# Kernel optimization log

Hardware: AMD Instinct MI355X
Metric: run time of the kernel (lower is better)

The kernel has to match this reference:

```python
import jax, jax.numpy as jnp
import numpy as np

N, E = 50000, 800000
D = 64          # output_dim == d_s == d_e
H = 128         # psi hidden width
PSI_IN = 2 * D + 2 * D + D  # 320


def setup_inputs() -> dict:
    key = jax.random.key(0)
    ks = jax.random.split(key, 12)
    scale = lambda fan_in: 1.0 / np.sqrt(fan_in)
    return {
        "h_d_prev": jax.random.normal(ks[0], (N, D), jnp.float32),
        "h_s": jax.random.normal(ks[1], (N, D), jnp.float32),
        "edge_feat": jax.random.normal(ks[2], (E, D), jnp.float32),
        "sender": jax.random.randint(ks[3], (E,), 0, N, jnp.int32),
        "receiver": jax.random.randint(ks[4], (E,), 0, N, jnp.int32),
        # psi MLP params (all layers use relu, incl. last: final_activation=None)
        "W0": jax.random.normal(ks[5], (PSI_IN, H), jnp.float32) * scale(PSI_IN),
        "b0": jnp.zeros((H,), jnp.float32),
        "W1": jax.random.normal(ks[6], (H, H), jnp.float32) * scale(H),
        "b1": jnp.zeros((H,), jnp.float32),
        "W2": jax.random.normal(ks[7], (H, D), jnp.float32) * scale(H),
        "b2": jnp.zeros((D,), jnp.float32),
        # final linear transform W (no bias)
        "Wm": jax.random.normal(ks[8], (D, D), jnp.float32) * scale(D),
    }


def reference(h_d_prev, h_s, edge_feat, sender, receiver, W0, b0, W1, b1, W2, b2, Wm):
    # gather node feats to edges
    h_di = h_d_prev[sender]      # [E, D]
    h_dj = h_d_prev[receiver]    # [E, D]
    h_si = h_s[sender]           # [E, D]
    h_sj = h_s[receiver]         # [E, D]
    psi_in = jnp.concatenate([h_si, h_sj, h_di, h_dj, edge_feat], axis=-1)  # [E, 320]
    # psi MLP: relu on every layer (final_activation=None keeps default relu)
    x = jax.nn.relu(psi_in @ W0 + b0)
    x = jax.nn.relu(x @ W1 + b1)
    psi = jax.nn.relu(x @ W2 + b2)          # [E, D]
    s_ij = psi * (h_dj - h_di)              # [E, D]
    agg = jax.ops.segment_sum(s_ij, receiver, num_segments=h_d_prev.shape[0])  # [N, D]
    return h_d_prev + agg @ Wm
```

## Files before the change

kernel.cpp:

```cpp
#include <hip/hip_runtime.h>

#define NN   50000
#define EE   800000
#define DD   64
#define HH   128
#define KIN  320
#define TILE_E 64

typedef __bf16 bf16x8 __attribute__((ext_vector_type(8)));
typedef float  f32x4  __attribute__((ext_vector_type(4)));

#if __has_builtin(__builtin_amdgcn_cvt_pk_bf16_f32)
typedef __bf16 bf16x2_t __attribute__((ext_vector_type(2)));
__device__ __forceinline__ unsigned int pk2(float a, float b) {
  union { bf16x2_t v; unsigned int u; } cv;
  cv.v = __builtin_amdgcn_cvt_pk_bf16_f32(a, b);
  return cv.u;
}
__device__ __forceinline__ unsigned short f2bf(float a) {
  return (unsigned short)(pk2(a, a) & 0xFFFFu);
}
#else
__device__ __forceinline__ unsigned short f2bf(float f) {
  union { float f; unsigned int u; } v; v.f = f;
  unsigned int u = v.u + 0x7FFFu + ((v.u >> 16) & 1u);
  return (unsigned short)(u >> 16);
}
__device__ __forceinline__ unsigned int pk2(float a, float b) {
  return (unsigned int)f2bf(a) | ((unsigned int)f2bf(b) << 16);
}
#endif

__device__ __forceinline__ float bf2f(unsigned short b) {
  union { unsigned int u; float f; } v; v.u = ((unsigned int)b) << 16; return v.f;
}

__device__ __forceinline__ int psiIdx(int row, int kk) {
  return ((((row >> 4) * 10 + (kk >> 5)) << 6) + ((row & 15) << 2) + ((kk >> 3) & 3)) * 8
         + (kk & 7);
}

__global__ __launch_bounds__(256) void prep_weights(
    const float* __restrict__ W0,
    const float* __restrict__ W1,
    const float* __restrict__ W2,
    unsigned short* __restrict__ WT0,
    unsigned short* __restrict__ WT1,
    unsigned short* __restrict__ WT2) {
  int t = blockIdx.x * 256 + threadIdx.x;
  if (t < KIN * HH) {
    int k = t / HH, n = t % HH;
    WT0[n * KIN + k] = f2bf(W0[t]);
  } else if (t < KIN * HH + HH * HH) {
    int u = t - KIN * HH; int k = u / HH, n = u % HH;
    WT1[n * HH + k] = f2bf(W1[u]);
  } else {
    int u = t - KIN * HH - HH * HH; int k = u / DD, n = u % DD;
    WT2[n * HH + k] = f2bf(W2[u]);
  }
}

__global__ __launch_bounds__(256) void prep_tables(
    const float* __restrict__ hd, const float* __restrict__ hs,
    unsigned short* __restrict__ hdb, unsigned short* __restrict__ hsb) {
  int t = blockIdx.x * 256 + threadIdx.x;
  const int n = NN * DD / 8;
  const float* src; unsigned short* dst; int i;
  if (t < n) { src = hd; dst = hdb; i = t; }
  else       { src = hs; dst = hsb; i = t - n; }
  float4 a = *(const float4*)(src + (size_t)i * 8);
  float4 b = *(const float4*)(src + (size_t)i * 8 + 4);
  uint4 w;
  w.x = pk2(a.x, a.y); w.y = pk2(a.z, a.w);
  w.z = pk2(b.x, b.y); w.w = pk2(b.z, b.w);
  *(uint4*)(dst + (size_t)i * 8) = w;
}

__global__ __launch_bounds__(256, 4) void edge_mlp(
    const unsigned short* __restrict__ hdb,
    const unsigned short* __restrict__ hsb,
    const float* __restrict__ ef,
    const int* __restrict__ snd,
    const int* __restrict__ rcv,
    const unsigned short* __restrict__ WT0,
    const float* __restrict__ b0,
    const unsigned short* __restrict__ WT1,
    const float* __restrict__ b1,
    const unsigned short* __restrict__ WT2,
    const float* __restrict__ b2,
    float* __restrict__ agg)
{
  __shared__ __align__(16) unsigned short psi[TILE_E * KIN];

  const int tid  = threadIdx.x;
  const int e0   = blockIdx.x * TILE_E;
  const int wv   = tid >> 6;
  const int lane = tid & 63;
  const int ln   = lane & 15;
  const int quad = lane >> 4;

  int ridx[16];
  #pragma unroll
  for (int mt = 0; mt < 4; ++mt)
    #pragma unroll
    for (int i = 0; i < 4; ++i)
      ridx[mt * 4 + i] = rcv[e0 + mt * 16 + quad * 4 + i];

  #pragma unroll
  for (int i = 0; i < 10; ++i) {
    const int seg = i >> 1;
    int e = ((i << 5) + (tid >> 3)) & 63;
    int c = tid & 7;
    int unit = (((e >> 4) * 10 + seg * 2 + (c >> 2)) << 6) + ((e & 15) << 2) + (c & 3);
    uint4 w;
    if (seg < 4) {
      const unsigned short* tb = (seg & 2) ? hdb : hsb;
      const int* ix = (seg & 1) ? rcv : snd;
      w = *(const uint4*)(tb + (size_t)ix[e0 + e] * DD + c * 8);
    } else {
      const float* src = ef + (size_t)(e0 + e) * DD;
      float4 v0 = *(const float4*)(src + c * 8);
      float4 v1 = *(const float4*)(src + c * 8 + 4);
      w.x = pk2(v0.x, v0.y); w.y = pk2(v0.z, v0.w);
      w.z = pk2(v1.x, v1.y); w.w = pk2(v1.z, v1.w);
    }
    *(uint4*)(&psi[unit * 8]) = w;
  }
  __syncthreads();

  f32x4 acc0[4], acc1[4];

  {
    #pragma unroll
    for (int m = 0; m < 4; ++m) { acc0[m] = (f32x4){0,0,0,0}; acc1[m] = (f32x4){0,0,0,0}; }
    const unsigned short* wb0 = WT0 + (wv * 32 + ln) * KIN + quad * 8;
    const unsigned short* wb1 = wb0 + 16 * KIN;
    #pragma unroll
    for (int k0 = 0; k0 < 10; ++k0) {
      bf16x8 bf0 = *(const bf16x8*)(wb0 + k0 * 32);
      bf16x8 bf1 = *(const bf16x8*)(wb1 + k0 * 32);
      #pragma unroll
      for (int mt = 0; mt < 4; ++mt) {
        bf16x8 af = *(const bf16x8*)(&psi[(((mt * 10 + k0) << 6) + (ln << 2) + quad) * 8]);
        acc0[mt] = __builtin_amdgcn_mfma_f32_16x16x32_bf16(af, bf0, acc0[mt], 0, 0, 0);
        acc1[mt] = __builtin_amdgcn_mfma_f32_16x16x32_bf16(af, bf1, acc1[mt], 0, 0, 0);
      }
    }
  }
  __syncthreads();

  {
    float bv0 = b0[wv * 32 + ln];
    float bv1 = b0[wv * 32 + 16 + ln];
    #pragma unroll
    for (int mt = 0; mt < 4; ++mt) {
      #pragma unroll
      for (int i = 0; i < 4; ++i) {
        int base = ((mt * 10 + wv) << 6) + ((quad * 4 + i) << 2) + (ln >> 3);
        float v0 = acc0[mt][i] + bv0; v0 = v0 > 0.f ? v0 : 0.f;
        float v1 = acc1[mt][i] + bv1; v1 = v1 > 0.f ? v1 : 0.f;
        psi[base * 8 + (ln & 7)]       = f2bf(v0);
        psi[(base + 2) * 8 + (ln & 7)] = f2bf(v1);
      }
    }
  }
  __syncthreads();

  {
    #pragma unroll
    for (int m = 0; m < 4; ++m) { acc0[m] = (f32x4){0,0,0,0}; acc1[m] = (f32x4){0,0,0,0}; }
    const unsigned short* wb0 = WT1 + (wv * 32 + ln) * HH + quad * 8;
    const unsigned short* wb1 = wb0 + 16 * HH;
    #pragma unroll
    for (int k0 = 0; k0 < 4; ++k0) {
      bf16x8 bf0 = *(const bf16x8*)(wb0 + k0 * 32);
      bf16x8 bf1 = *(const bf16x8*)(wb1 + k0 * 32);
      #pragma unroll
      for (int mt = 0; mt < 4; ++mt) {
        bf16x8 af = *(const bf16x8*)(&psi[(((mt * 10 + k0) << 6) + (ln << 2) + quad) * 8]);
        acc0[mt] = __builtin_amdgcn_mfma_f32_16x16x32_bf16(af, bf0, acc0[mt], 0, 0, 0);
        acc1[mt] = __builtin_amdgcn_mfma_f32_16x16x32_bf16(af, bf1, acc1[mt], 0, 0, 0);
      }
    }
  }
  __syncthreads();

  {
    float bv0 = b1[wv * 32 + ln];
    float bv1 = b1[wv * 32 + 16 + ln];
    #pragma unroll
    for (int mt = 0; mt < 4; ++mt) {
      #pragma unroll
      for (int i = 0; i < 4; ++i) {
        int base = ((mt * 10 + wv) << 6) + ((quad * 4 + i) << 2) + (ln >> 3);
        float v0 = acc0[mt][i] + bv0; v0 = v0 > 0.f ? v0 : 0.f;
        float v1 = acc1[mt][i] + bv1; v1 = v1 > 0.f ? v1 : 0.f;
        psi[base * 8 + (ln & 7)]       = f2bf(v0);
        psi[(base + 2) * 8 + (ln & 7)] = f2bf(v1);
      }
    }
  }
  __syncthreads();

  {
    f32x4 acc[4];
    #pragma unroll
    for (int m = 0; m < 4; ++m) acc[m] = (f32x4){0,0,0,0};
    const unsigned short* wb = WT2 + (wv * 16 + ln) * HH + quad * 8;
    #pragma unroll
    for (int k0 = 0; k0 < 4; ++k0) {
      bf16x8 bf = *(const bf16x8*)(wb + k0 * 32);
      #pragma unroll
      for (int mt = 0; mt < 4; ++mt) {
        bf16x8 af = *(const bf16x8*)(&psi[(((mt * 10 + k0) << 6) + (ln << 2) + quad) * 8]);
        acc[mt] = __builtin_amdgcn_mfma_f32_16x16x32_bf16(af, bf, acc[mt], 0, 0, 0);
      }
    }
    int   col = wv * 16 + ln;
    float bv  = b2[col];
    #pragma unroll
    for (int mt = 0; mt < 4; ++mt) {
      #pragma unroll
      for (int i = 0; i < 4; ++i) {
        int row = mt * 16 + quad * 4 + i;
        float p  = acc[mt][i] + bv; p = p > 0.f ? p : 0.f;
        float di = bf2f(psi[psiIdx(row, 128 + col)]);
        float dj = bf2f(psi[psiIdx(row, 192 + col)]);
        float s  = p * (dj - di);
        atomicAdd(&agg[(size_t)ridx[mt * 4 + i] * DD + col], s);
      }
    }
  }
}

__global__ __launch_bounds__(256) void final_out(
    const float* __restrict__ hd,
    const float* __restrict__ agg,
    const float* __restrict__ Wm,
    float* __restrict__ out)
{
  __shared__ float wmf[DD * DD];
  __shared__ float arow[16 * 72];
  int tid = threadIdx.x;
  const float4* wm4 = (const float4*)Wm;
  float4* wf4 = (float4*)wmf;
  #pragma unroll
  for (int i = tid; i < DD * DD / 4; i += 256) wf4[i] = wm4[i];

  int r0 = blockIdx.x * 16;
  {
    float4 av = *(const float4*)(agg + (size_t)r0 * DD + tid * 4);
    int rr = tid >> 4, cc = (tid & 15) * 4;
    *(float4*)&arow[rr * 72 + cc] = av;
  }
  __syncthreads();

  int row = tid >> 4;
  int cq  = (tid & 15) * 4;
  f32x4 acc = (f32x4){0, 0, 0, 0};
  #pragma unroll
  for (int k = 0; k < DD; ++k) {
    float a = arow[row * 72 + k];
    f32x4 w = *(const f32x4*)&wmf[k * DD + cq];
    acc += a * w;
  }
  size_t o = ((size_t)(r0 + row)) * DD + cq;
  f32x4 h = *(const f32x4*)(hd + o);
  *(f32x4*)(out + o) = h + acc;
}

extern "C" void kernel_launch(void* const* d_in, const int* in_sizes, int n_in,
                              void* d_out, int out_size, void* d_ws, size_t ws_size,
                              hipStream_t stream) {
  const float* hd = (const float*)d_in[0];
  const float* hs = (const float*)d_in[1];
  const float* ef = (const float*)d_in[2];
  const int* snd  = (const int*)d_in[3];
  const int* rcv  = (const int*)d_in[4];
  const float* W0 = (const float*)d_in[5];
  const float* b0 = (const float*)d_in[6];
  const float* W1 = (const float*)d_in[7];
  const float* b1 = (const float*)d_in[8];
  const float* W2 = (const float*)d_in[9];
  const float* b2 = (const float*)d_in[10];
  const float* Wm = (const float*)d_in[11];
  float* out      = (float*)d_out;

  char* ws = (char*)d_ws;
  float* agg = (float*)ws;
  unsigned short* WT0 = (unsigned short*)(ws + 12800000);
  unsigned short* WT1 = WT0 + KIN * HH;
  unsigned short* WT2 = WT1 + HH * HH;
  unsigned short* hdb = WT2 + HH * DD;
  unsigned short* hsb = hdb + (size_t)NN * DD;
  hipMemsetAsync(agg, 0, (size_t)NN * DD * sizeof(float), stream);
  prep_weights<<<256, 256, 0, stream>>>(W0, W1, W2, WT0, WT1, WT2);
  prep_tables<<<NN * DD * 2 / 8 / 256, 256, 0, stream>>>(hd, hs, hdb, hsb);
  edge_mlp<<<EE / TILE_E, 256, 0, stream>>>(hdb, hsb, ef, snd, rcv,
                                            WT0, b0, WT1, b1, WT2, b2, agg);
  final_out<<<NN / 16, 256, 0, stream>>>(hd, agg, Wm, out);
}
```

Measured before the change: 536.4 us.

## Halve edge tile to 32 and XOR-swizzle LDS staging layout

Shrinks the per-block edge tile from 64 to 32 edges, halving shared memory, accumulator and receiver-index registers, and raises the launch-bounds occupancy hint from 4 to 8 blocks. It also adds an XOR swizzle on the 16-byte unit index in the LDS staging buffer to reduce bank conflicts on the transposed activation writes and MFMA operand reads. The cost is that each weight fragment loaded from global/L2 is reused over half as many edge rows, so weight traffic per edge doubles, and the tighter register limit could cause spills.

```diff
diff --git a/kernel.cpp b/kernel.cpp
--- a/kernel.cpp
+++ b/kernel.cpp
@@ -5,7 +5,7 @@
 #define DD   64
 #define HH   128
 #define KIN  320
-#define TILE_E 64
+#define TILE_E 32
 
 typedef __bf16 bf16x8 __attribute__((ext_vector_type(8)));
 typedef float  f32x4  __attribute__((ext_vector_type(4)));
@@ -35,9 +35,12 @@
   union { unsigned int u; float f; } v; v.u = ((unsigned int)b) << 16; return v.f;
 }
 
+__device__ __forceinline__ int uaddr(int unit) {
+  return (unit ^ ((unit >> 4) & 3)) * 8;
+}
 __device__ __forceinline__ int psiIdx(int row, int kk) {
-  return ((((row >> 4) * 10 + (kk >> 5)) << 6) + ((row & 15) << 2) + ((kk >> 3) & 3)) * 8
-         + (kk & 7);
+  int unit = (((row >> 4) * 10 + (kk >> 5)) << 6) + ((row & 15) << 2) + ((kk >> 3) & 3);
+  return uaddr(unit) + (kk & 7);
 }
 
 __global__ __launch_bounds__(256) void prep_weights(
@@ -76,7 +79,7 @@
   *(uint4*)(dst + (size_t)i * 8) = w;
 }
 
-__global__ __launch_bounds__(256, 4) void edge_mlp(
+__global__ __launch_bounds__(256, 8) void edge_mlp(
     const unsigned short* __restrict__ hdb,
     const unsigned short* __restrict__ hsb,
     const float* __restrict__ ef,
@@ -99,40 +102,41 @@
   const int ln   = lane & 15;
   const int quad = lane >> 4;
 
-  int ridx[16];
+  int ridx[8];
   #pragma unroll
-  for (int mt = 0; mt < 4; ++mt)
+  for (int mt = 0; mt < 2; ++mt)
     #pragma unroll
     for (int i = 0; i < 4; ++i)
       ridx[mt * 4 + i] = rcv[e0 + mt * 16 + quad * 4 + i];
 
-  #pragma unroll
-  for (int i = 0; i < 10; ++i) {
-    const int seg = i >> 1;
-    int e = ((i << 5) + (tid >> 3)) & 63;
-    int c = tid & 7;
-    int unit = (((e >> 4) * 10 + seg * 2 + (c >> 2)) << 6) + ((e & 15) << 2) + (c & 3);
-    uint4 w;
-    if (seg < 4) {
-      const unsigned short* tb = (seg & 2) ? hdb : hsb;
-      const int* ix = (seg & 1) ? rcv : snd;
-      w = *(const uint4*)(tb + (size_t)ix[e0 + e] * DD + c * 8);
-    } else {
-      const float* src = ef + (size_t)(e0 + e) * DD;
-      float4 v0 = *(const float4*)(src + c * 8);
-      float4 v1 = *(const float4*)(src + c * 8 + 4);
-      w.x = pk2(v0.x, v0.y); w.y = pk2(v0.z, v0.w);
-      w.z = pk2(v1.x, v1.y); w.w = pk2(v1.z, v1.w);
-    }
-    *(uint4*)(&psi[unit * 8]) = w;
-  }
-  __syncthreads();
-
-  f32x4 acc0[4], acc1[4];
-
-  {
-    #pragma unroll
-    for (int m = 0; m < 4; ++m) { acc0[m] = (f32x4){0,0,0,0}; acc1[m] = (f32x4){0,0,0,0}; }
+  {
+    const int e = tid >> 3;
+    const int c = tid & 7;
+    #pragma unroll
+    for (int seg = 0; seg < 5; ++seg) {
+      int unit = (((e >> 4) * 10 + seg * 2 + (c >> 2)) << 6) + ((e & 15) << 2) + (c & 3);
+      uint4 w;
+      if (seg < 4) {
+        const unsigned short* tb = (seg & 2) ? hdb : hsb;
+        const int* ix = (seg & 1) ? rcv : snd;
+        w = *(const uint4*)(tb + (size_t)ix[e0 + e] * DD + c * 8);
+      } else {
+        const float* src = ef + (size_t)(e0 + e) * DD;
+        float4 v0 = *(const float4*)(src + c * 8);
+        float4 v1 = *(const float4*)(src + c * 8 + 4);
+        w.x = pk2(v0.x, v0.y); w.y = pk2(v0.z, v0.w);
+        w.z = pk2(v1.x, v1.y); w.w = pk2(v1.z, v1.w);
+      }
+      *(uint4*)(&psi[uaddr(unit)]) = w;
+    }
+  }
+  __syncthreads();
+
+  f32x4 acc0[2], acc1[2];
+
+  {
+    #pragma unroll
+    for (int m = 0; m < 2; ++m) { acc0[m] = (f32x4){0,0,0,0}; acc1[m] = (f32x4){0,0,0,0}; }
     const unsigned short* wb0 = WT0 + (wv * 32 + ln) * KIN + quad * 8;
     const unsigned short* wb1 = wb0 + 16 * KIN;
     #pragma unroll
@@ -140,8 +144,8 @@
       bf16x8 bf0 = *(const bf16x8*)(wb0 + k0 * 32);
       bf16x8 bf1 = *(const bf16x8*)(wb1 + k0 * 32);
       #pragma unroll
-      for (int mt = 0; mt < 4; ++mt) {
-        bf16x8 af = *(const bf16x8*)(&psi[(((mt * 10 + k0) << 6) + (ln << 2) + quad) * 8]);
+      for (int mt = 0; mt < 2; ++mt) {
+        bf16x8 af = *(const bf16x8*)(&psi[uaddr(((mt * 10 + k0) << 6) + (ln << 2) + quad)]);
         acc0[mt] = __builtin_amdgcn_mfma_f32_16x16x32_bf16(af, bf0, acc0[mt], 0, 0, 0);
         acc1[mt] = __builtin_amdgcn_mfma_f32_16x16x32_bf16(af, bf1, acc1[mt], 0, 0, 0);
       }
@@ -153,22 +157,22 @@
     float bv0 = b0[wv * 32 + ln];
     float bv1 = b0[wv * 32 + 16 + ln];
     #pragma unroll
-    for (int mt = 0; mt < 4; ++mt) {
+    for (int mt = 0; mt < 2; ++mt) {
       #pragma unroll
       for (int i = 0; i < 4; ++i) {
         int base = ((mt * 10 + wv) << 6) + ((quad * 4 + i) << 2) + (ln >> 3);
         float v0 = acc0[mt][i] + bv0; v0 = v0 > 0.f ? v0 : 0.f;
         float v1 = acc1[mt][i] + bv1; v1 = v1 > 0.f ? v1 : 0.f;
-        psi[base * 8 + (ln & 7)]       = f2bf(v0);
-        psi[(base + 2) * 8 + (ln & 7)] = f2bf(v1);
-      }
-    }
-  }
-  __syncthreads();
-
-  {
-    #pragma unroll
-    for (int m = 0; m < 4; ++m) { acc0[m] = (f32x4){0,0,0,0}; acc1[m] = (f32x4){0,0,0,0}; }
+        psi[uaddr(base)     + (ln & 7)] = f2bf(v0);
+        psi[uaddr(base + 2) + (ln & 7)] = f2bf(v1);
+      }
+    }
+  }
+  __syncthreads();
+
+  {
+    #pragma unroll
+    for (int m = 0; m < 2; ++m) { acc0[m] = (f32x4){0,0,0,0}; acc1[m] = (f32x4){0,0,0,0}; }
     const unsigned short* wb0 = WT1 + (wv * 32 + ln) * HH + quad * 8;
     const unsigned short* wb1 = wb0 + 16 * HH;
     #pragma unroll
@@ -176,8 +180,8 @@
       bf16x8 bf0 = *(const bf16x8*)(wb0 + k0 * 32);
       bf16x8 bf1 = *(const bf16x8*)(wb1 + k0 * 32);
       #pragma unroll
-      for (int mt = 0; mt < 4; ++mt) {
-        bf16x8 af = *(const bf16x8*)(&psi[(((mt * 10 + k0) << 6) + (ln << 2) + quad) * 8]);
+      for (int mt = 0; mt < 2; ++mt) {
+        bf16x8 af = *(const bf16x8*)(&psi[uaddr(((mt * 10 + k0) << 6) + (ln << 2) + quad)]);
         acc0[mt] = __builtin_amdgcn_mfma_f32_16x16x32_bf16(af, bf0, acc0[mt], 0, 0, 0);
         acc1[mt] = __builtin_amdgcn_mfma_f32_16x16x32_bf16(af, bf1, acc1[mt], 0, 0, 0);
       }
@@ -189,37 +193,37 @@
     float bv0 = b1[wv * 32 + ln];
     float bv1 = b1[wv * 32 + 16 + ln];
     #pragma unroll
-    for (int mt = 0; mt < 4; ++mt) {
+    for (int mt = 0; mt < 2; ++mt) {
       #pragma unroll
       for (int i = 0; i < 4; ++i) {
         int base = ((mt * 10 + wv) << 6) + ((quad * 4 + i) << 2) + (ln >> 3);
         float v0 = acc0[mt][i] + bv0; v0 = v0 > 0.f ? v0 : 0.f;
         float v1 = acc1[mt][i] + bv1; v1 = v1 > 0.f ? v1 : 0.f;
-        psi[base * 8 + (ln & 7)]       = f2bf(v0);
-        psi[(base + 2) * 8 + (ln & 7)] = f2bf(v1);
-      }
-    }
-  }
-  __syncthreads();
-
-  {
-    f32x4 acc[4];
-    #pragma unroll
-    for (int m = 0; m < 4; ++m) acc[m] = (f32x4){0,0,0,0};
+        psi[uaddr(base)     + (ln & 7)] = f2bf(v0);
+        psi[uaddr(base + 2) + (ln & 7)] = f2bf(v1);
+      }
+    }
+  }
+  __syncthreads();
+
+  {
+    f32x4 acc[2];
+    #pragma unroll
+    for (int m = 0; m < 2; ++m) acc[m] = (f32x4){0,0,0,0};
     const unsigned short* wb = WT2 + (wv * 16 + ln) * HH + quad * 8;
     #pragma unroll
     for (int k0 = 0; k0 < 4; ++k0) {
       bf16x8 bf = *(const bf16x8*)(wb + k0 * 32);
       #pragma unroll
-      for (int mt = 0; mt < 4; ++mt) {
-        bf16x8 af = *(const bf16x8*)(&psi[(((mt * 10 + k0) << 6) + (ln << 2) + quad) * 8]);
+      for (int mt = 0; mt < 2; ++mt) {
+        bf16x8 af = *(const bf16x8*)(&psi[uaddr(((mt * 10 + k0) << 6) + (ln << 2) + quad)]);
         acc[mt] = __builtin_amdgcn_mfma_f32_16x16x32_bf16(af, bf, acc[mt], 0, 0, 0);
       }
     }
     int   col = wv * 16 + ln;
     float bv  = b2[col];
     #pragma unroll
-    for (int mt = 0; mt < 4; ++mt) {
+    for (int mt = 0; mt < 2; ++mt) {
       #pragma unroll
       for (int i = 0; i < 4; ++i) {
         int row = mt * 16 + quad * 4 + i;
```

After: 789.1 us. 47.1% more time.

## Counting-sort edges by receiver and segment-reduce in tile before atomics

Applied to the files above, without the earlier changes.

Adds a counting sort of edges by receiver: a histogram in prep_tables, a single-block prefix scan, and a scatter that builds permuted edge, receiver and sender arrays. edge_mlp then processes edges in receiver order. It stages the per-edge messages in shared memory and does a run-length segmented sum per column, so there is one atomicAdd per distinct receiver instead of one per edge. This is meant to cut the ~51M global float atomics and improve locality of the receiver-side gathers. In exchange it adds three extra passes, a serial single-block scan, and edge_feat reads that go through the permutation instead of being sequential.

```diff
diff --git a/kernel.cpp b/kernel.cpp
--- a/kernel.cpp
+++ b/kernel.cpp
@@ -62,8 +62,10 @@
 
 __global__ __launch_bounds__(256) void prep_tables(
     const float* __restrict__ hd, const float* __restrict__ hs,
-    unsigned short* __restrict__ hdb, unsigned short* __restrict__ hsb) {
+    unsigned short* __restrict__ hdb, unsigned short* __restrict__ hsb,
+    const int* __restrict__ rcv, int* __restrict__ cnt) {
   int t = blockIdx.x * 256 + threadIdx.x;
+  atomicAdd(&cnt[rcv[t]], 1);
   const int n = NN * DD / 8;
   const float* src; unsigned short* dst; int i;
   if (t < n) { src = hd; dst = hdb; i = t; }
@@ -76,12 +78,47 @@
   *(uint4*)(dst + (size_t)i * 8) = w;
 }
 
+__global__ __launch_bounds__(1024) void scan_bins(int* __restrict__ cnt) {
+  __shared__ int ts[1024];
+  const int C = 49;
+  int t = threadIdx.x;
+  int base = t * C;
+  int s = 0;
+  for (int i = 0; i < C; ++i) { int idx = base + i; if (idx < NN) s += cnt[idx]; }
+  ts[t] = s;
+  __syncthreads();
+  for (int d = 1; d < 1024; d <<= 1) {
+    int v = (t >= d) ? ts[t - d] : 0;
+    __syncthreads();
+    ts[t] += v;
+    __syncthreads();
+  }
+  int run = (t == 0) ? 0 : ts[t - 1];
+  for (int i = 0; i < C; ++i) {
+    int idx = base + i;
+    if (idx < NN) { int c = cnt[idx]; cnt[idx] = run; run += c; }
+  }
+}
+
+__global__ __launch_bounds__(256) void scatter_perm(
+    const int* __restrict__ snd, const int* __restrict__ rcv,
+    const int* __restrict__ cnt, int* __restrict__ cursor,
+    int* __restrict__ perm, int* __restrict__ rsorted, int* __restrict__ ssorted) {
+  int e = blockIdx.x * 256 + threadIdx.x;
+  int r = rcv[e];
+  int pos = cnt[r] + atomicAdd(&cursor[r], 1);
+  perm[pos]    = e;
+  rsorted[pos] = r;
+  ssorted[pos] = snd[e];
+}
+
 __global__ __launch_bounds__(256, 4) void edge_mlp(
     const unsigned short* __restrict__ hdb,
     const unsigned short* __restrict__ hsb,
     const float* __restrict__ ef,
-    const int* __restrict__ snd,
-    const int* __restrict__ rcv,
+    const int* __restrict__ perm,
+    const int* __restrict__ rsorted,
+    const int* __restrict__ ssorted,
     const unsigned short* __restrict__ WT0,
     const float* __restrict__ b0,
     const unsigned short* __restrict__ WT1,
@@ -99,12 +136,8 @@
   const int ln   = lane & 15;
   const int quad = lane >> 4;
 
-  int ridx[16];
-  #pragma unroll
-  for (int mt = 0; mt < 4; ++mt)
-    #pragma unroll
-    for (int i = 0; i < 4; ++i)
-      ridx[mt * 4 + i] = rcv[e0 + mt * 16 + quad * 4 + i];
+  int myr = 0;
+  if (tid < TILE_E) myr = rsorted[e0 + tid];
 
   #pragma unroll
   for (int i = 0; i < 10; ++i) {
@@ -115,10 +148,11 @@
     uint4 w;
     if (seg < 4) {
       const unsigned short* tb = (seg & 2) ? hdb : hsb;
-      const int* ix = (seg & 1) ? rcv : snd;
+      const int* ix = (seg & 1) ? rsorted : ssorted;
       w = *(const uint4*)(tb + (size_t)ix[e0 + e] * DD + c * 8);
     } else {
-      const float* src = ef + (size_t)(e0 + e) * DD;
+      int re = perm[e0 + e];
+      const float* src = ef + (size_t)re * DD;
       float4 v0 = *(const float4*)(src + c * 8);
       float4 v1 = *(const float4*)(src + c * 8 + 4);
       w.x = pk2(v0.x, v0.y); w.y = pk2(v0.z, v0.w);
@@ -218,6 +252,7 @@
     }
     int   col = wv * 16 + ln;
     float bv  = b2[col];
+    float sv[16];
     #pragma unroll
     for (int mt = 0; mt < 4; ++mt) {
       #pragma unroll
@@ -226,10 +261,41 @@
         float p  = acc[mt][i] + bv; p = p > 0.f ? p : 0.f;
         float di = bf2f(psi[psiIdx(row, 128 + col)]);
         float dj = bf2f(psi[psiIdx(row, 192 + col)]);
-        float s  = p * (dj - di);
-        atomicAdd(&agg[(size_t)ridx[mt * 4 + i] * DD + col], s);
-      }
-    }
+        sv[mt * 4 + i] = p * (dj - di);
+      }
+    }
+    __syncthreads();
+
+    float* st = (float*)psi;
+    int*   rt = (int*)(psi + 8192);
+    #pragma unroll
+    for (int mt = 0; mt < 4; ++mt) {
+      #pragma unroll
+      for (int i = 0; i < 4; ++i) {
+        int row = mt * 16 + quad * 4 + i;
+        st[row * 64 + (col ^ (quad << 3))] = sv[mt * 4 + i];
+      }
+    }
+    if (tid < TILE_E) rt[tid] = myr;
+    __syncthreads();
+
+    int c2  = tid & 63;
+    int rr0 = (tid >> 6) * 16;
+    float a  = 0.f;
+    int  prev = rt[rr0];
+    #pragma unroll
+    for (int j = 0; j < 16; ++j) {
+      int row = rr0 + j;
+      int rc  = rt[row];
+      float v = st[row * 64 + (c2 ^ ((((unsigned)row >> 2) & 3) << 3))];
+      if (rc != prev) {
+        atomicAdd(&agg[(size_t)prev * DD + c2], a);
+        a = v; prev = rc;
+      } else {
+        a += v;
+      }
+    }
+    atomicAdd(&agg[(size_t)prev * DD + c2], a);
   }
 }
 
@@ -287,16 +353,24 @@
   float* out      = (float*)d_out;
 
   char* ws = (char*)d_ws;
-  float* agg = (float*)ws;
-  unsigned short* WT0 = (unsigned short*)(ws + 12800000);
+  float* agg  = (float*)ws;
+  int* cnt    = (int*)(ws + 12800000);
+  int* cursor = (int*)(ws + 13000000);
+  unsigned short* WT0 = (unsigned short*)(ws + 13200000);
   unsigned short* WT1 = WT0 + KIN * HH;
   unsigned short* WT2 = WT1 + HH * HH;
-  unsigned short* hdb = WT2 + HH * DD;
+  int* perm    = (int*)(ws + 13331072);
+  int* rsorted = perm + EE;
+  int* ssorted = rsorted + EE;
+  unsigned short* hdb = (unsigned short*)(ssorted + EE);
   unsigned short* hsb = hdb + (size_t)NN * DD;
-  hipMemsetAsync(agg, 0, (size_t)NN * DD * sizeof(float), stream);
+  hipMemsetAsync(ws, 0, 13200000, stream);
   prep_weights<<<256, 256, 0, stream>>>(W0, W1, W2, WT0, WT1, WT2);
-  prep_tables<<<NN * DD * 2 / 8 / 256, 256, 0, stream>>>(hd, hs, hdb, hsb);
-  edge_mlp<<<EE / TILE_E, 256, 0, stream>>>(hdb, hsb, ef, snd, rcv,
+  prep_tables<<<NN * DD * 2 / 8 / 256, 256, 0, stream>>>(hd, hs, hdb, hsb, rcv, cnt);
+  scan_bins<<<1, 1024, 0, stream>>>(cnt);
+  scatter_perm<<<EE / 256, 256, 0, stream>>>(snd, rcv, cnt, cursor,
+                                             perm, rsorted, ssorted);
+  edge_mlp<<<EE / TILE_E, 256, 0, stream>>>(hdb, hsb, ef, perm, rsorted, ssorted,
                                             WT0, b0, WT1, b1, WT2, b2, agg);
   final_out<<<NN / 16, 256, 0, stream>>>(hd, agg, Wm, out);
 }
```

Result: slower. 683.1 us (+27.4%).

## Double edge tile to 128 with 512 threads, register-cached weights, fused prep kernels

Applied to the files above, without the earlier changes.

The edge MLP now handles 128 edges per block with 8 waves. Each wave owns one 16-column slice across all 8 row tiles and keeps its weight fragments in registers, with the gathers for both edge halves issued before any LDS store. The memset, weight conversion and table conversion are merged into one prep kernel, removing launch overhead. The aim is more gather memory-level parallelism and better weight reuse, at the cost of higher register pressure under launch_bounds(512,4) and double the LDS per block.

```diff
diff --git a/kernel.cpp b/kernel.cpp
--- a/kernel.cpp
+++ b/kernel.cpp
@@ -5,7 +5,7 @@
 #define DD   64
 #define HH   128
 #define KIN  320
-#define TILE_E 64
+#define TILE_E 128
 
 typedef __bf16 bf16x8 __attribute__((ext_vector_type(8)));
 typedef float  f32x4  __attribute__((ext_vector_type(4)));
@@ -40,43 +40,43 @@
          + (kk & 7);
 }
 
-__global__ __launch_bounds__(256) void prep_weights(
-    const float* __restrict__ W0,
-    const float* __restrict__ W1,
+__global__ __launch_bounds__(256) void prep_all(
+    const float* __restrict__ hd, const float* __restrict__ hs,
+    const float* __restrict__ W0, const float* __restrict__ W1,
     const float* __restrict__ W2,
-    unsigned short* __restrict__ WT0,
-    unsigned short* __restrict__ WT1,
-    unsigned short* __restrict__ WT2) {
-  int t = blockIdx.x * 256 + threadIdx.x;
-  if (t < KIN * HH) {
-    int k = t / HH, n = t % HH;
-    WT0[n * KIN + k] = f2bf(W0[t]);
-  } else if (t < KIN * HH + HH * HH) {
-    int u = t - KIN * HH; int k = u / HH, n = u % HH;
-    WT1[n * HH + k] = f2bf(W1[u]);
+    unsigned short* __restrict__ hdb, unsigned short* __restrict__ hsb,
+    unsigned short* __restrict__ WT0, unsigned short* __restrict__ WT1,
+    unsigned short* __restrict__ WT2, float* __restrict__ agg) {
+  int b = blockIdx.x;
+  int t = b * 256 + threadIdx.x;
+  if (b < 3125) {
+    *(float4*)(agg + (size_t)t * 4) = (float4){0.f, 0.f, 0.f, 0.f};
+    const int n = NN * DD / 8;
+    const float* src; unsigned short* dst; int i;
+    if (t < n) { src = hd; dst = hdb; i = t; }
+    else       { src = hs; dst = hsb; i = t - n; }
+    float4 a = *(const float4*)(src + (size_t)i * 8);
+    float4 c = *(const float4*)(src + (size_t)i * 8 + 4);
+    uint4 w;
+    w.x = pk2(a.x, a.y); w.y = pk2(a.z, a.w);
+    w.z = pk2(c.x, c.y); w.w = pk2(c.z, c.w);
+    *(uint4*)(dst + (size_t)i * 8) = w;
   } else {
-    int u = t - KIN * HH - HH * HH; int k = u / DD, n = u % DD;
-    WT2[n * HH + k] = f2bf(W2[u]);
-  }
-}
-
-__global__ __launch_bounds__(256) void prep_tables(
-    const float* __restrict__ hd, const float* __restrict__ hs,
-    unsigned short* __restrict__ hdb, unsigned short* __restrict__ hsb) {
-  int t = blockIdx.x * 256 + threadIdx.x;
-  const int n = NN * DD / 8;
-  const float* src; unsigned short* dst; int i;
-  if (t < n) { src = hd; dst = hdb; i = t; }
-  else       { src = hs; dst = hsb; i = t - n; }
-  float4 a = *(const float4*)(src + (size_t)i * 8);
-  float4 b = *(const float4*)(src + (size_t)i * 8 + 4);
-  uint4 w;
-  w.x = pk2(a.x, a.y); w.y = pk2(a.z, a.w);
-  w.z = pk2(b.x, b.y); w.w = pk2(b.z, b.w);
-  *(uint4*)(dst + (size_t)i * 8) = w;
-}
-
-__global__ __launch_bounds__(256, 4) void edge_mlp(
+    int u = t - 3125 * 256;
+    if (u < KIN * HH) {
+      int k = u / HH, n2 = u % HH;
+      WT0[n2 * KIN + k] = f2bf(W0[u]);
+    } else if (u < KIN * HH + HH * HH) {
+      int v = u - KIN * HH; int k = v / HH, n2 = v % HH;
+      WT1[n2 * HH + k] = f2bf(W1[v]);
+    } else {
+      int v = u - KIN * HH - HH * HH; int k = v / DD, n2 = v % DD;
+      WT2[n2 * HH + k] = f2bf(W2[v]);
+    }
+  }
+}
+
+__global__ __launch_bounds__(512, 4) void edge_mlp(
     const unsigned short* __restrict__ hdb,
     const unsigned short* __restrict__ hsb,
     const float* __restrict__ ef,
@@ -98,138 +98,145 @@
   const int lane = tid & 63;
   const int ln   = lane & 15;
   const int quad = lane >> 4;
+  const int mtb  = (wv >> 2) * 4;
 
   int ridx[16];
   #pragma unroll
   for (int mt = 0; mt < 4; ++mt)
     #pragma unroll
     for (int i = 0; i < 4; ++i)
-      ridx[mt * 4 + i] = rcv[e0 + mt * 16 + quad * 4 + i];
-
-  #pragma unroll
-  for (int i = 0; i < 10; ++i) {
-    const int seg = i >> 1;
-    int e = ((i << 5) + (tid >> 3)) & 63;
-    int c = tid & 7;
-    int unit = (((e >> 4) * 10 + seg * 2 + (c >> 2)) << 6) + ((e & 15) << 2) + (c & 3);
-    uint4 w;
-    if (seg < 4) {
-      const unsigned short* tb = (seg & 2) ? hdb : hsb;
-      const int* ix = (seg & 1) ? rcv : snd;
-      w = *(const uint4*)(tb + (size_t)ix[e0 + e] * DD + c * 8);
-    } else {
-      const float* src = ef + (size_t)(e0 + e) * DD;
-      float4 v0 = *(const float4*)(src + c * 8);
-      float4 v1 = *(const float4*)(src + c * 8 + 4);
-      w.x = pk2(v0.x, v0.y); w.y = pk2(v0.z, v0.w);
-      w.z = pk2(v1.x, v1.y); w.w = pk2(v1.z, v1.w);
-    }
-    *(uint4*)(&psi[unit * 8]) = w;
-  }
-  __syncthreads();
-
-  f32x4 acc0[4], acc1[4];
-
-  {
-    #pragma unroll
-    for (int m = 0; m < 4; ++m) { acc0[m] = (f32x4){0,0,0,0}; acc1[m] = (f32x4){0,0,0,0}; }
-    const unsigned short* wb0 = WT0 + (wv * 32 + ln) * KIN + quad * 8;
-    const unsigned short* wb1 = wb0 + 16 * KIN;
-    #pragma unroll
-    for (int k0 = 0; k0 < 10; ++k0) {
-      bf16x8 bf0 = *(const bf16x8*)(wb0 + k0 * 32);
-      bf16x8 bf1 = *(const bf16x8*)(wb1 + k0 * 32);
-      #pragma unroll
-      for (int mt = 0; mt < 4; ++mt) {
-        bf16x8 af = *(const bf16x8*)(&psi[(((mt * 10 + k0) << 6) + (ln << 2) + quad) * 8]);
-        acc0[mt] = __builtin_amdgcn_mfma_f32_16x16x32_bf16(af, bf0, acc0[mt], 0, 0, 0);
-        acc1[mt] = __builtin_amdgcn_mfma_f32_16x16x32_bf16(af, bf1, acc1[mt], 0, 0, 0);
-      }
-    }
-  }
-  __syncthreads();
-
-  {
-    float bv0 = b0[wv * 32 + ln];
-    float bv1 = b0[wv * 32 + 16 + ln];
-    #pragma unroll
-    for (int mt = 0; mt < 4; ++mt) {
-      #pragma unroll
-      for (int i = 0; i < 4; ++i) {
-        int base = ((mt * 10 + wv) << 6) + ((quad * 4 + i) << 2) + (ln >> 3);
-        float v0 = acc0[mt][i] + bv0; v0 = v0 > 0.f ? v0 : 0.f;
-        float v1 = acc1[mt][i] + bv1; v1 = v1 > 0.f ? v1 : 0.f;
-        psi[base * 8 + (ln & 7)]       = f2bf(v0);
-        psi[(base + 2) * 8 + (ln & 7)] = f2bf(v1);
-      }
-    }
-  }
-  __syncthreads();
-
-  {
-    #pragma unroll
-    for (int m = 0; m < 4; ++m) { acc0[m] = (f32x4){0,0,0,0}; acc1[m] = (f32x4){0,0,0,0}; }
-    const unsigned short* wb0 = WT1 + (wv * 32 + ln) * HH + quad * 8;
-    const unsigned short* wb1 = wb0 + 16 * HH;
-    #pragma unroll
-    for (int k0 = 0; k0 < 4; ++k0) {
-      bf16x8 bf0 = *(const bf16x8*)(wb0 + k0 * 32);
-      bf16x8 bf1 = *(const bf16x8*)(wb1 + k0 * 32);
-      #pragma unroll
-      for (int mt = 0; mt < 4; ++mt) {
-        bf16x8 af = *(const bf16x8*)(&psi[(((mt * 10 + k0) << 6) + (ln << 2) + quad) * 8]);
-        acc0[mt] = __builtin_amdgcn_mfma_f32_16x16x32_bf16(af, bf0, acc0[mt], 0, 0, 0);
-        acc1[mt] = __builtin_amdgcn_mfma_f32_16x16x32_bf16(af, bf1, acc1[mt], 0, 0, 0);
-      }
-    }
-  }
-  __syncthreads();
-
-  {
-    float bv0 = b1[wv * 32 + ln];
-    float bv1 = b1[wv * 32 + 16 + ln];
-    #pragma unroll
-    for (int mt = 0; mt < 4; ++mt) {
-      #pragma unroll
-      for (int i = 0; i < 4; ++i) {
-        int base = ((mt * 10 + wv) << 6) + ((quad * 4 + i) << 2) + (ln >> 3);
-        float v0 = acc0[mt][i] + bv0; v0 = v0 > 0.f ? v0 : 0.f;
-        float v1 = acc1[mt][i] + bv1; v1 = v1 > 0.f ? v1 : 0.f;
-        psi[base * 8 + (ln & 7)]       = f2bf(v0);
-        psi[(base + 2) * 8 + (ln & 7)] = f2bf(v1);
-      }
-    }
-  }
-  __syncthreads();
-
-  {
-    f32x4 acc[4];
-    #pragma unroll
-    for (int m = 0; m < 4; ++m) acc[m] = (f32x4){0,0,0,0};
-    const unsigned short* wb = WT2 + (wv * 16 + ln) * HH + quad * 8;
-    #pragma unroll
-    for (int k0 = 0; k0 < 4; ++k0) {
-      bf16x8 bf = *(const bf16x8*)(wb + k0 * 32);
-      #pragma unroll
-      for (int mt = 0; mt < 4; ++mt) {
-        bf16x8 af = *(const bf16x8*)(&psi[(((mt * 10 + k0) << 6) + (ln << 2) + quad) * 8]);
-        acc[mt] = __builtin_amdgcn_mfma_f32_16x16x32_bf16(af, bf, acc[mt], 0, 0, 0);
-      }
-    }
-    int   col = wv * 16 + ln;
-    float bv  = b2[col];
-    #pragma unroll
-    for (int mt = 0; mt < 4; ++mt) {
+      ridx[mt * 4 + i] = rcv[e0 + (mtb + mt) * 16 + quad * 4 + i];
+
+  {
+    const int eA = tid >> 3;
+    const int eB = eA + 64;
+    const int c  = tid & 7;
+    const int siA = snd[e0 + eA], siB = snd[e0 + eB];
+    const int riA = rcv[e0 + eA], riB = rcv[e0 + eB];
+    uint4 w[10];
+    #pragma unroll
+    for (int i = 0; i < 10; ++i) {
+      const int seg = i >> 1;
+      if (seg < 4) {
+        const unsigned short* tb = (seg & 2) ? hdb : hsb;
+        int ix = (seg & 1) ? ((i & 1) ? riB : riA)
+                           : ((i & 1) ? siB : siA);
+        w[i] = *(const uint4*)(tb + (size_t)ix * DD + c * 8);
+      } else {
+        const int e = (i & 1) ? eB : eA;
+        const float* src = ef + (size_t)(e0 + e) * DD + c * 8;
+        float4 v0 = *(const float4*)(src);
+        float4 v1 = *(const float4*)(src + 4);
+        w[i].x = pk2(v0.x, v0.y); w[i].y = pk2(v0.z, v0.w);
+        w[i].z = pk2(v1.x, v1.y); w[i].w = pk2(v1.z, v1.w);
+      }
+    }
+    #pragma unroll
+    for (int i = 0; i < 10; ++i) {
+      const int seg = i >> 1;
+      const int e   = (i & 1) ? eB : eA;
+      int unit = (((e >> 4) * 10 + seg * 2 + (c >> 2)) << 6) + ((e & 15) << 2) + (c & 3);
+      *(uint4*)(&psi[unit * 8]) = w[i];
+    }
+  }
+
+  const int col = wv * 16 + ln;
+
+  bf16x8 wf[10];
+  {
+    const unsigned short* wb = WT0 + col * KIN + quad * 8;
+    #pragma unroll
+    for (int k0 = 0; k0 < 10; ++k0) wf[k0] = *(const bf16x8*)(wb + k0 * 32);
+  }
+  __syncthreads();
+
+  f32x4 acc[8];
+
+  #pragma unroll
+  for (int m = 0; m < 8; ++m) acc[m] = (f32x4){0,0,0,0};
+  #pragma unroll
+  for (int k0 = 0; k0 < 10; ++k0)
+    #pragma unroll
+    for (int mt = 0; mt < 8; ++mt) {
+      bf16x8 af = *(const bf16x8*)(&psi[(((mt * 10 + k0) << 6) + (ln << 2) + quad) * 8]);
+      acc[mt] = __builtin_amdgcn_mfma_f32_16x16x32_bf16(af, wf[k0], acc[mt], 0, 0, 0);
+    }
+  __syncthreads();
+
+  {
+    float bv = b0[col];
+    #pragma unroll
+    for (int mt = 0; mt < 8; ++mt)
       #pragma unroll
       for (int i = 0; i < 4; ++i) {
         int row = mt * 16 + quad * 4 + i;
-        float p  = acc[mt][i] + bv; p = p > 0.f ? p : 0.f;
-        float di = bf2f(psi[psiIdx(row, 128 + col)]);
-        float dj = bf2f(psi[psiIdx(row, 192 + col)]);
+        float v = acc[mt][i] + bv; v = v > 0.f ? v : 0.f;
+        psi[psiIdx(row, col)] = f2bf(v);
+      }
+  }
+  bf16x8 wg[4];
+  {
+    const unsigned short* wb = WT1 + col * HH + quad * 8;
+    #pragma unroll
+    for (int k0 = 0; k0 < 4; ++k0) wg[k0] = *(const bf16x8*)(wb + k0 * 32);
+  }
+  __syncthreads();
+
+  #pragma unroll
+  for (int m = 0; m < 8; ++m) acc[m] = (f32x4){0,0,0,0};
+  #pragma unroll
+  for (int k0 = 0; k0 < 4; ++k0)
+    #pragma unroll
+    for (int mt = 0; mt < 8; ++mt) {
+      bf16x8 af = *(const bf16x8*)(&psi[(((mt * 10 + k0) << 6) + (ln << 2) + quad) * 8]);
+      acc[mt] = __builtin_amdgcn_mfma_f32_16x16x32_bf16(af, wg[k0], acc[mt], 0, 0, 0);
+    }
+  __syncthreads();
+
+  {
+    float bv = b1[col];
+    #pragma unroll
+    for (int mt = 0; mt < 8; ++mt)
+      #pragma unroll
+      for (int i = 0; i < 4; ++i) {
+        int row = mt * 16 + quad * 4 + i;
+        float v = acc[mt][i] + bv; v = v > 0.f ? v : 0.f;
+        psi[psiIdx(row, col)] = f2bf(v);
+      }
+  }
+  const int col2 = (wv & 3) * 16 + ln;
+  bf16x8 wh[4];
+  {
+    const unsigned short* wb = WT2 + col2 * HH + quad * 8;
+    #pragma unroll
+    for (int k0 = 0; k0 < 4; ++k0) wh[k0] = *(const bf16x8*)(wb + k0 * 32);
+  }
+  __syncthreads();
+
+  {
+    f32x4 acc2[4];
+    #pragma unroll
+    for (int m = 0; m < 4; ++m) acc2[m] = (f32x4){0,0,0,0};
+    #pragma unroll
+    for (int k0 = 0; k0 < 4; ++k0)
+      #pragma unroll
+      for (int m = 0; m < 4; ++m) {
+        int mt = mtb + m;
+        bf16x8 af = *(const bf16x8*)(&psi[(((mt * 10 + k0) << 6) + (ln << 2) + quad) * 8]);
+        acc2[m] = __builtin_amdgcn_mfma_f32_16x16x32_bf16(af, wh[k0], acc2[m], 0, 0, 0);
+      }
+    float bv = b2[col2];
+    #pragma unroll
+    for (int m = 0; m < 4; ++m)
+      #pragma unroll
+      for (int i = 0; i < 4; ++i) {
+        int row = (mtb + m) * 16 + quad * 4 + i;
+        float p  = acc2[m][i] + bv; p = p > 0.f ? p : 0.f;
+        float di = bf2f(psi[psiIdx(row, 128 + col2)]);
+        float dj = bf2f(psi[psiIdx(row, 192 + col2)]);
         float s  = p * (dj - di);
-        atomicAdd(&agg[(size_t)ridx[mt * 4 + i] * DD + col], s);
-      }
-    }
+        atomicAdd(&agg[(size_t)ridx[m * 4 + i] * DD + col2], s);
+      }
   }
 }
 
@@ -293,10 +300,9 @@
   unsigned short* WT2 = WT1 + HH * HH;
   unsigned short* hdb = WT2 + HH * DD;
   unsigned short* hsb = hdb + (size_t)NN * DD;
-  hipMemsetAsync(agg, 0, (size_t)NN * DD * sizeof(float), stream);
-  prep_weights<<<256, 256, 0, stream>>>(W0, W1, W2, WT0, WT1, WT2);
-  prep_tables<<<NN * DD * 2 / 8 / 256, 256, 0, stream>>>(hd, hs, hdb, hsb);
-  edge_mlp<<<EE / TILE_E, 256, 0, stream>>>(hdb, hsb, ef, snd, rcv,
+  prep_all<<<3381, 256, 0, stream>>>(hd, hs, W0, W1, W2,
+                                     hdb, hsb, WT0, WT1, WT2, agg);
+  edge_mlp<<<EE / TILE_E, 512, 0, stream>>>(hdb, hsb, ef, snd, rcv,
                                             WT0, b0, WT1, b1, WT2, b2, agg);
   final_out<<<NN / 16, 256, 0, stream>>>(hd, agg, Wm, out);
 }
```

Result: faster. 521.0 us (-2.9%).
